# Kernel optimization log

Measured on AMD Instinct MI355X. Metric: run time of the kernel, lower is better.

Reference implementation:

```python
import jax, jax.numpy as jnp
import numpy as np

B, T, C = 256, 2048, 39   # batch, time, nb_filters
NB = 8                     # number of dilation levels (2**0 .. 2**7)
K = 2                      # kernel size
NC = 8                     # num_classes
EPS = 1e-5                 # BatchNorm eps (eval mode)


def _causal_conv(x, w, b, d):
    """x: [B,C,T], w: [Cout,Cin,K], left-pad (K-1)*d for causality."""
    k = w.shape[-1]
    y = jax.lax.conv_general_dilated(
        x, w, window_strides=(1,), padding=[((k - 1) * d, 0)],
        rhs_dilation=(d,), dimension_numbers=('NCH', 'OIH', 'NCH'))
    return y + b[None, :, None]


def _bn(x, g, be, m, v):
    # eval-mode BatchNorm1d with running stats
    return g[None, :, None] * (x - m[None, :, None]) * jax.lax.rsqrt(v + EPS)[None, :, None] + be[None, :, None]


def _block(x, w, b, g, be, m, v, d):
    # Temporal_Aware_Block, eval mode (dropout = identity).
    # w: [2,C,C,K], b/g/be/m/v: [2,C]
    y = jax.nn.relu(_bn(_causal_conv(x, w[0], b[0], d), g[0], be[0], m[0], v[0]))
    y = jax.nn.relu(_bn(_causal_conv(y, w[1], b[1], d), g[1], be[1], m[1], v[1]))
    # causal conv preserves length, so the 1x1 residual conv branch is never taken
    return x * jax.nn.sigmoid(y)


def setup_inputs() -> dict:
    key = jax.random.key(0)
    ks = jax.random.split(key, 24)
    f = lambda k, s: jax.random.normal(k, s, dtype=jnp.float32) * 0.1
    return {
        'inputs': jax.random.normal(ks[0], (B, T, C), dtype=jnp.float32),
        'conv1x1_w': f(ks[1], (C, C, 1)),
        'conv1x1_b': f(ks[2], (C,)),
        'fw_conv_w': f(ks[3], (NB, 2, C, C, K)),
        'fw_conv_b': f(ks[4], (NB, 2, C)),
        'fw_gamma': 1.0 + f(ks[5], (NB, 2, C)),
        'fw_beta': f(ks[6], (NB, 2, C)),
        'fw_mean': f(ks[7], (NB, 2, C)),
        'fw_var': jax.random.uniform(ks[8], (NB, 2, C), dtype=jnp.float32, minval=0.5, maxval=1.5),
        'bw_conv_w': f(ks[9], (NB, 2, C, C, K)),
        'bw_conv_b': f(ks[10], (NB, 2, C)),
        'bw_gamma': 1.0 + f(ks[11], (NB, 2, C)),
        'bw_beta': f(ks[12], (NB, 2, C)),
        'bw_mean': f(ks[13], (NB, 2, C)),
        'bw_var': jax.random.uniform(ks[14], (NB, 2, C), dtype=jnp.float32, minval=0.5, maxval=1.5),
        'wl_kernel': f(ks[15], (NB, 1)),
        'cls_w': f(ks[16], (NC, C)),
        'cls_b': f(ks[17], (NC,)),
    }


def reference(inputs, conv1x1_w, conv1x1_b,
              fw_conv_w, fw_conv_b, fw_gamma, fw_beta, fw_mean, fw_var,
              bw_conv_w, bw_conv_b, bw_gamma, bw_beta, bw_mean, bw_var,
              wl_kernel, cls_w, cls_b):
    x = jnp.transpose(inputs, (0, 2, 1))           # [B,C,T]
    fwd = _causal_conv(x, conv1x1_w, conv1x1_b, 1)
    bwd = _causal_conv(x[:, :, ::-1], conv1x1_w, conv1x1_b, 1)
    skips = []
    for i in range(NB):
        d = 2 ** i
        fwd = _block(fwd, fw_conv_w[i], fw_conv_b[i], fw_gamma[i], fw_beta[i], fw_mean[i], fw_var[i], d)
        bwd = _block(bwd, bw_conv_w[i], bw_conv_b[i], bw_gamma[i], bw_beta[i], bw_mean[i], bw_var[i], d)
        skips.append(jnp.mean(fwd + bwd, axis=-1))  # [B,C]
    g = jnp.stack(skips, axis=-1)                   # [B,C,NB]
    x2 = jnp.einsum('bcn,no->bc', g, wl_kernel)     # WeightLayer matmul + squeeze
    logits = x2 @ cls_w.T + cls_b                   # [B,NC]
    return jax.nn.log_softmax(logits, axis=1)
```

## Files before the change

### kernel.cpp

```cpp
#include <hip/hip_runtime.h>
#include <math.h>

#define BATCH 256
#define TT    2048
#define CC    39
#define CP    40
#define Y1ST  44
#define NBLK  8
#define KK    2
#define NCLS  8
#define BN_EPS 1e-5f

typedef __attribute__((ext_vector_type(8))) short short8;
typedef __attribute__((ext_vector_type(4))) float floatx4;

__device__ __forceinline__ unsigned short f2b(float f) {
    union { float f; unsigned u; } v; v.f = f;
    unsigned r = v.u + 0x7FFF + ((v.u >> 16) & 1);
    return (unsigned short)(r >> 16);
}
__device__ __forceinline__ unsigned cvtpk(float lo, float hi) {
    unsigned r;
    asm("v_cvt_pk_bf16_f32 %0, %1, %2" : "=v"(r) : "v"(lo), "v"(hi));
    return r;
}
__device__ __forceinline__ float blo(unsigned u) {
    union { unsigned v; float f; } k; k.v = u << 16; return k.f;
}
__device__ __forceinline__ float bhi(unsigned u) {
    union { unsigned v; float f; } k; k.v = u & 0xffff0000u; return k.f;
}
__device__ __forceinline__ void gl_lds16(const void* g, void* l) {
    __builtin_amdgcn_global_load_lds(
        (const __attribute__((address_space(1))) unsigned int*)g,
        (__attribute__((address_space(3))) unsigned int*)l, 16, 0, 0);
}

#define WFB_PER   (2*3*3*512)
#define WFB_TOTAL (2*NBLK*WFB_PER)
#define BFB_TOTAL (2*NBLK*2*48)
#define WFF_TOTAL (3*2*512)
#define BFF_TOTAL 48
#define ZPAD_SHORTS (256 * CP)

__global__ void fold_kernel(const float* __restrict__ fw_w, const float* __restrict__ fw_b,
                            const float* __restrict__ fw_g, const float* __restrict__ fw_be,
                            const float* __restrict__ fw_m, const float* __restrict__ fw_v,
                            const float* __restrict__ bw_w, const float* __restrict__ bw_b,
                            const float* __restrict__ bw_g, const float* __restrict__ bw_be,
                            const float* __restrict__ bw_m, const float* __restrict__ bw_v,
                            const float* __restrict__ c1w, const float* __restrict__ c1b,
                            unsigned short* __restrict__ wfb, float* __restrict__ bfb,
                            unsigned short* __restrict__ wff, float* __restrict__ bff) {
    int idx = blockIdx.x * blockDim.x + threadIdx.x;
    if (idx < WFB_TOTAL) {
        int i = idx;
        int reg = i & 7;   i >>= 3;
        int lane = i & 63; i >>= 6;
        int sl = i % 3;    i /= 3;
        int ct = i % 3;    i /= 3;
        int layer = i & 1; i >>= 1;
        int blk = i & 7;   i >>= 3;
        int dir = i;
        int g = lane >> 4;
        int co = ct * 16 + (lane & 15);
        int p, ci; bool ok = true;
        if (sl < 2) {
            int kin = (g << 3) + reg;
            p = kin >> 4;
            ci = sl * 16 + (kin & 15);
        } else {
            p = g & 1;
            ci = 32 + reg;
            ok = (g < 2);
        }
        float val = 0.f;
        if (ok && co < CC && ci < CC) {
            const float* w = dir ? bw_w : fw_w;
            const float* gam = dir ? bw_g : fw_g;
            const float* var = dir ? bw_v : fw_v;
            int il = blk * 2 + layer;
            float sc = gam[il * CC + co] * rsqrtf(var[il * CC + co] + BN_EPS);
            val = w[((size_t)(il * CC + co) * CC + ci) * KK + p] * sc;
        }
        wfb[idx] = f2b(val);
        return;
    }
    idx -= WFB_TOTAL;
    if (idx < BFB_TOTAL) {
        int co = idx % 48;
        int i = idx / 48;
        int layer = i & 1; i >>= 1;
        int blk = i & 7;   i >>= 3;
        int dir = i;
        float val = 0.f;
        if (co < CC) {
            const float* b  = dir ? bw_b  : fw_b;
            const float* g  = dir ? bw_g  : fw_g;
            const float* be = dir ? bw_be : fw_be;
            const float* m  = dir ? bw_m  : fw_m;
            const float* v  = dir ? bw_v  : fw_v;
            int r = (blk * 2 + layer) * CC + co;
            float sc = g[r] * rsqrtf(v[r] + BN_EPS);
            val = (b[r] - m[r]) * sc + be[r];
        }
        bfb[idx] = val;
        return;
    }
    idx -= BFB_TOTAL;
    if (idx < WFF_TOTAL) {
        int i = idx;
        int reg = i & 7;   i >>= 3;
        int lane = i & 63; i >>= 6;
        int sl = i & 1;    i >>= 1;
        int ct = i;
        int co = ct * 16 + (lane & 15);
        int ci = sl * 32 + ((lane >> 4) << 3) + reg;
        float val = (co < CC && ci < CC) ? c1w[co * CC + ci] : 0.f;
        wff[idx] = f2b(val);
        return;
    }
    idx -= WFF_TOTAL;
    if (idx < BFF_TOTAL) {
        bff[idx] = (idx < CC) ? c1b[idx] : 0.f;
    }
}

__global__ __launch_bounds__(256) void front_mfma(const float* __restrict__ in,
                                                  const unsigned short* __restrict__ wf,
                                                  const float* __restrict__ bias,
                                                  unsigned short* __restrict__ out) {
    __shared__ unsigned short xt[256 * CP + 32];
    const int dir = blockIdx.z, b = blockIdx.y, t0 = blockIdx.x * 256;
    const int tid = threadIdx.x, lane = tid & 63, wave = tid >> 6;
    const int c = lane & 15, g = lane >> 4;
    const int stmin = dir ? (TT - t0 - 256) : t0;
    const float* src = in + ((size_t)b * TT + stmin) * CC;

    unsigned* xd = (unsigned*)xt;
    for (int e = tid; e < 256 * 20; e += 256) {
        int row = e / 20, cp = e - row * 20;
        int c0 = cp * 2;
        float f0 = src[(size_t)row * CC + c0];
        float f1 = (c0 + 1 < CC) ? src[(size_t)row * CC + c0 + 1] : 0.f;
        xd[row * 20 + cp] = cvtpk(f0, f1);
    }
    if (tid < 16) ((unsigned*)(xt + 256 * CP))[tid] = 0;
    __syncthreads();

    short8 Wf[3][2];
#pragma unroll
    for (int ct = 0; ct < 3; ++ct)
#pragma unroll
        for (int sl = 0; sl < 2; ++sl)
            Wf[ct][sl] = *(const short8*)(wf + (((ct * 2 + sl) * 64 + lane) << 3));
    float bs[3][4];
#pragma unroll
    for (int ct = 0; ct < 3; ++ct)
#pragma unroll
        for (int j = 0; j < 4; ++j) bs[ct][j] = bias[ct * 16 + g * 4 + j];

    for (int mt = wave; mt < 16; mt += 4) {
        int row = (mt << 4) + c;
        const unsigned short* bp = xt + row * CP;
        floatx4 acc[3];
#pragma unroll
        for (int ct = 0; ct < 3; ++ct)
            acc[ct] = floatx4{bs[ct][0], bs[ct][1], bs[ct][2], bs[ct][3]};
#pragma unroll
        for (int sl = 0; sl < 2; ++sl) {
            short8 B = *(const short8*)(bp + sl * 32 + g * 8);
#pragma unroll
            for (int ct = 0; ct < 3; ++ct)
                acc[ct] = __builtin_amdgcn_mfma_f32_16x16x32_bf16(Wf[ct][sl], B, acc[ct], 0, 0, 0);
        }
        int t = dir ? (t0 + 255 - row) : (t0 + row);
        unsigned short* op = out + ((size_t)(dir * BATCH + b) * TT + t) * CP;
#pragma unroll
        for (int ct = 0; ct < 3; ++ct) {
            if (ct == 2 && g >= 2) continue;
            uint2 v;
            v.x = cvtpk(acc[ct][0], acc[ct][1]);
            v.y = cvtpk(acc[ct][2], acc[ct][3]);
            *(uint2*)(op + ct * 16 + g * 4) = v;
        }
    }
}

template <int D, int TtC>
__global__ __launch_bounds__(256) void block_mfma(const unsigned short* __restrict__ xg,
                                                  unsigned short* __restrict__ yg,
                                                  const unsigned short* __restrict__ wf_all,
                                                  const float* __restrict__ bf_all,
                                                  float* __restrict__ skipPart,
                                                  const unsigned short* __restrict__ zpad,
                                                  int blk, int writeOut) {
    constexpr int ROWS_X   = TtC + 2 * D;
    constexpr int NCH      = ROWS_X * 5;
    constexpr int NIT      = (NCH + 255) / 256;
    constexpr int XT_SHORTS = NIT * 256 * 8;
    constexpr int M1       = (TtC + D + 15) / 16;
    constexpr int ROWS_Y1  = M1 * 16;
    constexpr int ROWS_REAL = TtC + D;
    constexpr int Y1_SHORTS = ROWS_Y1 * Y1ST + 8;
    constexpr int M2W      = TtC / 64;

    extern __shared__ char ldsraw[];
    unsigned short* xt = (unsigned short*)ldsraw;
    unsigned short* y1 = xt + XT_SHORTS;
    float* stash = (float*)(y1 + Y1_SHORTS);

    const int dir = blockIdx.z, b = blockIdx.y, tile = blockIdx.x;
    const int t0 = tile * TtC;
    const int tid = threadIdx.x, lane = tid & 63, wave = tid >> 6;
    const int c = lane & 15, g = lane >> 4;

    const size_t cbase = (size_t)(dir * BATCH + b) * TT * CP;
    const unsigned short* wf = wf_all + (size_t)(dir * NBLK + blk) * WFB_PER;
    const float* bf = bf_all + (size_t)(dir * NBLK + blk) * 96;

    {
        const unsigned short* gx = xg + cbase;
#pragma unroll
        for (int it = 0; it < NIT; ++it) {
            int chunk = it * 256 + wave * 64 + lane;
            unsigned row = (unsigned)chunk / 5u;
            int sub = chunk - (int)row * 5;
            int t = t0 - 2 * D + (int)row;
            const unsigned short* src = (chunk < NCH && t >= 0)
                ? (gx + (size_t)t * CP + sub * 8)
                : (zpad + ((row & 255u) * CP + sub * 8));
            unsigned short* dst = xt + (size_t)(it * 256 + wave * 64) * 8;
            gl_lds16(src, dst);
        }
    }

    short8 Wf[3][3];
#pragma unroll
    for (int ct = 0; ct < 3; ++ct)
#pragma unroll
        for (int sl = 0; sl < 3; ++sl)
            Wf[ct][sl] = *(const short8*)(wf + ((((0 * 3 + ct) * 3 + sl) * 64 + lane) << 3));
    float bs[3][4];
#pragma unroll
    for (int ct = 0; ct < 3; ++ct)
#pragma unroll
        for (int j = 0; j < 4; ++j) bs[ct][j] = bf[ct * 16 + g * 4 + j];

    __syncthreads();

    const int r01off = (g >> 1) * D;
    const int r2off  = (g & 1) * D;
    const int koff8  = (g & 1) << 3;

    for (int mt = wave; mt < M1; mt += 4) {
        int j0 = mt << 4;
        const unsigned short* bp01 = xt + (j0 + c + r01off) * CP + koff8;
        const unsigned short* bp2  = xt + (j0 + c + r2off) * CP + 32;
        short8 B0 = *(const short8*)(bp01);
        short8 B1 = *(const short8*)(bp01 + 16);
        short8 B2 = *(const short8*)(bp2);
        floatx4 acc[3];
#pragma unroll
        for (int ct = 0; ct < 3; ++ct) {
            acc[ct] = floatx4{bs[ct][0], bs[ct][1], bs[ct][2], bs[ct][3]};
            acc[ct] = __builtin_amdgcn_mfma_f32_16x16x32_bf16(Wf[ct][0], B0, acc[ct], 0, 0, 0);
            acc[ct] = __builtin_amdgcn_mfma_f32_16x16x32_bf16(Wf[ct][1], B1, acc[ct], 0, 0, 0);
            acc[ct] = __builtin_amdgcn_mfma_f32_16x16x32_bf16(Wf[ct][2], B2, acc[ct], 0, 0, 0);
        }
        int r = j0 + c;
        bool dead = (t0 - D + r < 0) || (r >= ROWS_REAL);
        unsigned short* yp = y1 + r * Y1ST;
#pragma unroll
        for (int ct = 0; ct < 3; ++ct) {
            if (ct == 2 && g >= 2) continue;
            uint2 v;
            v.x = cvtpk(fmaxf(acc[ct][0], 0.f), fmaxf(acc[ct][1], 0.f));
            v.y = cvtpk(fmaxf(acc[ct][2], 0.f), fmaxf(acc[ct][3], 0.f));
            if (dead) { v.x = 0u; v.y = 0u; }
            *(uint2*)(yp + ct * 16 + g * 4) = v;
        }
    }
    __syncthreads();

#pragma unroll
    for (int ct = 0; ct < 3; ++ct)
#pragma unroll
        for (int sl = 0; sl < 3; ++sl)
            Wf[ct][sl] = *(const short8*)(wf + ((((1 * 3 + ct) * 3 + sl) * 64 + lane) << 3));
#pragma unroll
    for (int ct = 0; ct < 3; ++ct)
#pragma unroll
        for (int j = 0; j < 4; ++j) bs[ct][j] = bf[48 + ct * 16 + g * 4 + j];

    float sums[3][4];
#pragma unroll
    for (int ct = 0; ct < 3; ++ct)
#pragma unroll
        for (int j = 0; j < 4; ++j) sums[ct][j] = 0.f;

#pragma unroll
    for (int mi = 0; mi < M2W; ++mi) {
        int j0 = (wave * M2W + mi) << 4;
        const unsigned short* bp01 = y1 + (j0 + c + r01off) * Y1ST + koff8;
        const unsigned short* bp2  = y1 + (j0 + c + r2off) * Y1ST + 32;
        short8 B0 = *(const short8*)(bp01);
        short8 B1 = *(const short8*)(bp01 + 16);
        short8 B2 = *(const short8*)(bp2);
        floatx4 acc[3];
#pragma unroll
        for (int ct = 0; ct < 3; ++ct) {
            acc[ct] = floatx4{bs[ct][0], bs[ct][1], bs[ct][2], bs[ct][3]};
            acc[ct] = __builtin_amdgcn_mfma_f32_16x16x32_bf16(Wf[ct][0], B0, acc[ct], 0, 0, 0);
            acc[ct] = __builtin_amdgcn_mfma_f32_16x16x32_bf16(Wf[ct][1], B1, acc[ct], 0, 0, 0);
            acc[ct] = __builtin_amdgcn_mfma_f32_16x16x32_bf16(Wf[ct][2], B2, acc[ct], 0, 0, 0);
        }
        int r = j0 + c;
        const unsigned short* xrow = xt + (r + 2 * D) * CP;
        unsigned short* orow = yg + cbase + (size_t)(t0 + r) * CP;
#pragma unroll
        for (int ct = 0; ct < 3; ++ct) {
            uint2 xv = *(const uint2*)(xrow + ct * 16 + g * 4);
            float g0 = blo(xv.x) * __builtin_amdgcn_rcpf(1.f + __expf(-acc[ct][0]));
            float g1 = bhi(xv.x) * __builtin_amdgcn_rcpf(1.f + __expf(-acc[ct][1]));
            float g2 = blo(xv.y) * __builtin_amdgcn_rcpf(1.f + __expf(-acc[ct][2]));
            float g3 = bhi(xv.y) * __builtin_amdgcn_rcpf(1.f + __expf(-acc[ct][3]));
            sums[ct][0] += g0; sums[ct][1] += g1;
            sums[ct][2] += g2; sums[ct][3] += g3;
            if (writeOut && !(ct == 2 && g >= 2)) {
                uint2 v;
                v.x = cvtpk(g0, g1);
                v.y = cvtpk(g2, g3);
                *(uint2*)(orow + ct * 16 + g * 4) = v;
            }
        }
    }
#pragma unroll
    for (int ct = 0; ct < 3; ++ct)
#pragma unroll
        for (int j = 0; j < 4; ++j) {
            float v = sums[ct][j];
            v += __shfl_xor(v, 1, 64);
            v += __shfl_xor(v, 2, 64);
            v += __shfl_xor(v, 4, 64);
            v += __shfl_xor(v, 8, 64);
            sums[ct][j] = v;
        }
    if (c == 0) {
#pragma unroll
        for (int ct = 0; ct < 3; ++ct)
#pragma unroll
            for (int j = 0; j < 4; ++j)
                stash[wave * 48 + ct * 16 + g * 4 + j] = sums[ct][j];
    }
    __syncthreads();
    if (tid < CC) {
        float s = stash[tid] + stash[48 + tid] + stash[96 + tid] + stash[144 + tid];
        skipPart[(((size_t)(blk * 2 + dir) * BATCH + b) * CC + tid) * 16 + tile] = s;
    }
}

static inline size_t lds_bytes_for(int D, int Tt) {
    int rows_x = Tt + 2 * D;
    int nch = rows_x * 5;
    int nit = (nch + 255) / 256;
    int xt_shorts = nit * 256 * 8;
    int m1 = (Tt + D + 15) / 16;
    int y1_shorts = m1 * 16 * Y1ST + 8;
    return (size_t)(xt_shorts + y1_shorts) * 2 + 192 * 4;
}

__global__ __launch_bounds__(64) void tail_kernel(const float* __restrict__ skipPart,
                                                  const float* __restrict__ wl,
                                                  const float* __restrict__ cw,
                                                  const float* __restrict__ cb,
                                                  float* __restrict__ out) {
    __shared__ float xs[CC];
    int b = blockIdx.x;
    int cth = threadIdx.x;
    if (cth < CC) {
        float x2 = 0.f;
        for (int i = 0; i < NBLK; ++i) {
            float wli = wl[i] * (1.0f / TT);
            int nt = (i == NBLK - 1) ? 16 : 8;
            for (int dirn = 0; dirn < 2; ++dirn) {
                const float* sp = skipPart + (((size_t)(i * 2 + dirn) * BATCH + b) * CC + cth) * 16;
                float s = 0.f;
                for (int tl = 0; tl < nt; ++tl) s += sp[tl];
                x2 = fmaf(s, wli, x2);
            }
        }
        xs[cth] = x2;
    }
    __syncthreads();
    if (threadIdx.x == 0) {
        float lg[NCLS];
        float mx = -1e30f;
        for (int o = 0; o < NCLS; ++o) {
            float a = cb[o];
#pragma unroll
            for (int cc2 = 0; cc2 < CC; ++cc2) a = fmaf(cw[o * CC + cc2], xs[cc2], a);
            lg[o] = a;
            mx = fmaxf(mx, a);
        }
        float se = 0.f;
        for (int o = 0; o < NCLS; ++o) se += expf(lg[o] - mx);
        float lse = logf(se) + mx;
        for (int o = 0; o < NCLS; ++o) out[b * NCLS + o] = lg[o] - lse;
    }
}

extern "C" void kernel_launch(void* const* d_in, const int* in_sizes, int n_in,
                              void* d_out, int out_size, void* d_ws, size_t ws_size,
                              hipStream_t stream) {
    const float* inputs = (const float*)d_in[0];
    const float* c1w    = (const float*)d_in[1];
    const float* c1b    = (const float*)d_in[2];
    const float* fw_w   = (const float*)d_in[3];
    const float* fw_b   = (const float*)d_in[4];
    const float* fw_g   = (const float*)d_in[5];
    const float* fw_be  = (const float*)d_in[6];
    const float* fw_m   = (const float*)d_in[7];
    const float* fw_v   = (const float*)d_in[8];
    const float* bw_w   = (const float*)d_in[9];
    const float* bw_b   = (const float*)d_in[10];
    const float* bw_g   = (const float*)d_in[11];
    const float* bw_be  = (const float*)d_in[12];
    const float* bw_m   = (const float*)d_in[13];
    const float* bw_v   = (const float*)d_in[14];
    const float* wl     = (const float*)d_in[15];
    const float* clsw   = (const float*)d_in[16];
    const float* clsb   = (const float*)d_in[17];

    const size_t bufsz = (size_t)2 * BATCH * TT * CP;
    unsigned short* buf0 = (unsigned short*)d_ws;
    unsigned short* buf1 = buf0 + bufsz;
    float* skip = (float*)(buf1 + bufsz);
    const size_t skipsz = (size_t)NBLK * 2 * BATCH * CC * 16;
    unsigned short* wfb = (unsigned short*)(skip + skipsz);
    float* bfb = (float*)(wfb + WFB_TOTAL);
    unsigned short* wff = (unsigned short*)(bfb + BFB_TOTAL);
    float* bff = (float*)(wff + WFF_TOTAL);
    unsigned short* zpad = (unsigned short*)(bff + BFF_TOTAL);

    hipMemsetAsync(zpad, 0, ZPAD_SHORTS * sizeof(unsigned short), stream);

    {
        int tot = WFB_TOTAL + BFB_TOTAL + WFF_TOTAL + BFF_TOTAL;
        fold_kernel<<<(tot + 255) / 256, 256, 0, stream>>>(
            fw_w, fw_b, fw_g, fw_be, fw_m, fw_v,
            bw_w, bw_b, bw_g, bw_be, bw_m, bw_v, c1w, c1b,
            wfb, bfb, wff, bff);
    }

    front_mfma<<<dim3(TT / 256, BATCH, 2), 256, 0, stream>>>(inputs, wff, bff, buf0);

    unsigned short* cur = buf0;
    unsigned short* nxt = buf1;
#define LAUNCH_BLOCK(DD, TTC)                                                        \
    block_mfma<DD, TTC><<<dim3(TT / TTC, BATCH, 2), 256, lds_bytes_for(DD, TTC),     \
                          stream>>>(cur, nxt, wfb, bfb, skip, zpad, i,               \
                                    (i < NBLK - 1) ? 1 : 0)
    for (int i = 0; i < NBLK; ++i) {
        switch (i) {
            case 0: LAUNCH_BLOCK(1, 256); break;
            case 1: LAUNCH_BLOCK(2, 256); break;
            case 2: LAUNCH_BLOCK(4, 256); break;
            case 3: LAUNCH_BLOCK(8, 256); break;
            case 4: LAUNCH_BLOCK(16, 256); break;
            case 5: LAUNCH_BLOCK(32, 256); break;
            case 6: LAUNCH_BLOCK(64, 256); break;
            case 7: LAUNCH_BLOCK(128, 128); break;
        }
        unsigned short* tmp = cur; cur = nxt; nxt = tmp;
    }
#undef LAUNCH_BLOCK

    tail_kernel<<<BATCH, 64, 0, stream>>>(skip, wl, clsw, clsb, (float*)d_out);
}
```

Before: 553.6 us.

## Use 512-thread blocks, share front conv across directions, unify tile size

The front 1x1 conv now runs once per batch/time tile and writes both the forward and the time-reversed copies, instead of launching a separate direction that redoes the same conv. The residual block kernel moves to 512 threads (8 waves), so each block has more waves to hide latency, and its LDS staging for x is sized exactly to the needed rows instead of being rounded up to whole load iterations. The last dilation level now also uses 256-step tiles, and the tail sums 8 partials per level. The risk is more LDS and registers per block at large dilations, which could lower occupancy, and the doubled, scattered writes in the front kernel.

```diff
diff --git a/kernel.cpp b/kernel.cpp
--- a/kernel.cpp
+++ b/kernel.cpp
@@ -10,6 +10,7 @@
 #define KK    2
 #define NCLS  8
 #define BN_EPS 1e-5f
+#define TBLK  512
 
 typedef __attribute__((ext_vector_type(8))) short short8;
 typedef __attribute__((ext_vector_type(4))) float floatx4;
@@ -131,11 +132,10 @@
                                                   const float* __restrict__ bias,
                                                   unsigned short* __restrict__ out) {
     __shared__ unsigned short xt[256 * CP + 32];
-    const int dir = blockIdx.z, b = blockIdx.y, t0 = blockIdx.x * 256;
+    const int b = blockIdx.y, t0 = blockIdx.x * 256;
     const int tid = threadIdx.x, lane = tid & 63, wave = tid >> 6;
     const int c = lane & 15, g = lane >> 4;
-    const int stmin = dir ? (TT - t0 - 256) : t0;
-    const float* src = in + ((size_t)b * TT + stmin) * CC;
+    const float* src = in + ((size_t)b * TT + t0) * CC;
 
     unsigned* xd = (unsigned*)xt;
     for (int e = tid; e < 256 * 20; e += 256) {
@@ -174,36 +174,39 @@
             for (int ct = 0; ct < 3; ++ct)
                 acc[ct] = __builtin_amdgcn_mfma_f32_16x16x32_bf16(Wf[ct][sl], B, acc[ct], 0, 0, 0);
         }
-        int t = dir ? (t0 + 255 - row) : (t0 + row);
-        unsigned short* op = out + ((size_t)(dir * BATCH + b) * TT + t) * CP;
+        int t = t0 + row;
+        unsigned short* op0 = out + ((size_t)b * TT + t) * CP;
+        unsigned short* op1 = out + ((size_t)(BATCH + b) * TT + (TT - 1 - t)) * CP;
 #pragma unroll
         for (int ct = 0; ct < 3; ++ct) {
             if (ct == 2 && g >= 2) continue;
             uint2 v;
             v.x = cvtpk(acc[ct][0], acc[ct][1]);
             v.y = cvtpk(acc[ct][2], acc[ct][3]);
-            *(uint2*)(op + ct * 16 + g * 4) = v;
+            *(uint2*)(op0 + ct * 16 + g * 4) = v;
+            *(uint2*)(op1 + ct * 16 + g * 4) = v;
         }
     }
 }
 
 template <int D, int TtC>
-__global__ __launch_bounds__(256) void block_mfma(const unsigned short* __restrict__ xg,
-                                                  unsigned short* __restrict__ yg,
-                                                  const unsigned short* __restrict__ wf_all,
-                                                  const float* __restrict__ bf_all,
-                                                  float* __restrict__ skipPart,
-                                                  const unsigned short* __restrict__ zpad,
-                                                  int blk, int writeOut) {
+__global__ __launch_bounds__(TBLK) void block_mfma(const unsigned short* __restrict__ xg,
+                                                   unsigned short* __restrict__ yg,
+                                                   const unsigned short* __restrict__ wf_all,
+                                                   const float* __restrict__ bf_all,
+                                                   float* __restrict__ skipPart,
+                                                   const unsigned short* __restrict__ zpad,
+                                                   int blk, int writeOut) {
+    constexpr int NW       = TBLK / 64;
     constexpr int ROWS_X   = TtC + 2 * D;
     constexpr int NCH      = ROWS_X * 5;
-    constexpr int NIT      = (NCH + 255) / 256;
-    constexpr int XT_SHORTS = NIT * 256 * 8;
+    constexpr int NIT      = (NCH + TBLK - 1) / TBLK;
+    constexpr int XT_SHORTS = ROWS_X * CP;
     constexpr int M1       = (TtC + D + 15) / 16;
     constexpr int ROWS_Y1  = M1 * 16;
     constexpr int ROWS_REAL = TtC + D;
     constexpr int Y1_SHORTS = ROWS_Y1 * Y1ST + 8;
-    constexpr int M2W      = TtC / 64;
+    constexpr int M2W      = TtC / (16 * NW);
 
     extern __shared__ char ldsraw[];
     unsigned short* xt = (unsigned short*)ldsraw;
@@ -223,15 +226,16 @@
         const unsigned short* gx = xg + cbase;
 #pragma unroll
         for (int it = 0; it < NIT; ++it) {
-            int chunk = it * 256 + wave * 64 + lane;
-            unsigned row = (unsigned)chunk / 5u;
-            int sub = chunk - (int)row * 5;
-            int t = t0 - 2 * D + (int)row;
-            const unsigned short* src = (chunk < NCH && t >= 0)
-                ? (gx + (size_t)t * CP + sub * 8)
-                : (zpad + ((row & 255u) * CP + sub * 8));
-            unsigned short* dst = xt + (size_t)(it * 256 + wave * 64) * 8;
-            gl_lds16(src, dst);
+            int chunk = it * TBLK + wave * 64 + lane;
+            if (chunk < NCH) {
+                unsigned row = (unsigned)chunk / 5u;
+                int sub = chunk - (int)row * 5;
+                int t = t0 - 2 * D + (int)row;
+                const unsigned short* src = (t >= 0)
+                    ? (gx + (size_t)t * CP + sub * 8)
+                    : (zpad + (row * CP + sub * 8));
+                gl_lds16(src, xt + (size_t)(it * TBLK + wave * 64) * 8);
+            }
         }
     }
 
@@ -253,7 +257,7 @@
     const int r2off  = (g & 1) * D;
     const int koff8  = (g & 1) << 3;
 
-    for (int mt = wave; mt < M1; mt += 4) {
+    for (int mt = wave; mt < M1; mt += NW) {
         int j0 = mt << 4;
         const unsigned short* bp01 = xt + (j0 + c + r01off) * CP + koff8;
         const unsigned short* bp2  = xt + (j0 + c + r2off) * CP + 32;
@@ -355,19 +359,19 @@
     }
     __syncthreads();
     if (tid < CC) {
-        float s = stash[tid] + stash[48 + tid] + stash[96 + tid] + stash[144 + tid];
+        float s = 0.f;
+#pragma unroll
+        for (int w = 0; w < NW; ++w) s += stash[w * 48 + tid];
         skipPart[(((size_t)(blk * 2 + dir) * BATCH + b) * CC + tid) * 16 + tile] = s;
     }
 }
 
 static inline size_t lds_bytes_for(int D, int Tt) {
     int rows_x = Tt + 2 * D;
-    int nch = rows_x * 5;
-    int nit = (nch + 255) / 256;
-    int xt_shorts = nit * 256 * 8;
+    int xt_shorts = rows_x * CP;
     int m1 = (Tt + D + 15) / 16;
     int y1_shorts = m1 * 16 * Y1ST + 8;
-    return (size_t)(xt_shorts + y1_shorts) * 2 + 192 * 4;
+    return (size_t)(xt_shorts + y1_shorts) * 2 + (TBLK / 64) * 48 * 4;
 }
 
 __global__ __launch_bounds__(64) void tail_kernel(const float* __restrict__ skipPart,
@@ -382,11 +386,11 @@
         float x2 = 0.f;
         for (int i = 0; i < NBLK; ++i) {
             float wli = wl[i] * (1.0f / TT);
-            int nt = (i == NBLK - 1) ? 16 : 8;
             for (int dirn = 0; dirn < 2; ++dirn) {
                 const float* sp = skipPart + (((size_t)(i * 2 + dirn) * BATCH + b) * CC + cth) * 16;
                 float s = 0.f;
-                for (int tl = 0; tl < nt; ++tl) s += sp[tl];
+#pragma unroll
+                for (int tl = 0; tl < 8; ++tl) s += sp[tl];
                 x2 = fmaf(s, wli, x2);
             }
         }
@@ -453,24 +457,24 @@
             wfb, bfb, wff, bff);
     }
 
-    front_mfma<<<dim3(TT / 256, BATCH, 2), 256, 0, stream>>>(inputs, wff, bff, buf0);
+    front_mfma<<<dim3(TT / 256, BATCH, 1), 256, 0, stream>>>(inputs, wff, bff, buf0);
 
     unsigned short* cur = buf0;
     unsigned short* nxt = buf1;
-#define LAUNCH_BLOCK(DD, TTC)                                                        \
-    block_mfma<DD, TTC><<<dim3(TT / TTC, BATCH, 2), 256, lds_bytes_for(DD, TTC),     \
+#define LAUNCH_BLOCK(DD)                                                             \
+    block_mfma<DD, 256><<<dim3(TT / 256, BATCH, 2), TBLK, lds_bytes_for(DD, 256),    \
                           stream>>>(cur, nxt, wfb, bfb, skip, zpad, i,               \
                                     (i < NBLK - 1) ? 1 : 0)
     for (int i = 0; i < NBLK; ++i) {
         switch (i) {
-            case 0: LAUNCH_BLOCK(1, 256); break;
-            case 1: LAUNCH_BLOCK(2, 256); break;
-            case 2: LAUNCH_BLOCK(4, 256); break;
-            case 3: LAUNCH_BLOCK(8, 256); break;
-            case 4: LAUNCH_BLOCK(16, 256); break;
-            case 5: LAUNCH_BLOCK(32, 256); break;
-            case 6: LAUNCH_BLOCK(64, 256); break;
-            case 7: LAUNCH_BLOCK(128, 128); break;
+            case 0: LAUNCH_BLOCK(1); break;
+            case 1: LAUNCH_BLOCK(2); break;
+            case 2: LAUNCH_BLOCK(4); break;
+            case 3: LAUNCH_BLOCK(8); break;
+            case 4: LAUNCH_BLOCK(16); break;
+            case 5: LAUNCH_BLOCK(32); break;
+            case 6: LAUNCH_BLOCK(64); break;
+            case 7: LAUNCH_BLOCK(128); break;
         }
         unsigned short* tmp = cur; cur = nxt; nxt = tmp;
     }
```

Result: no change. 554.4 us (+0.1%).
